# Kernel tuning notes

Hardware: AMD Instinct MI355X
Metric: run time of the kernel (lower is better)

## Reference

```python
import jax, jax.numpy as jnp
import numpy as np

EPS = 1e-5
SLOPE = 0.01  # LeakyReLU default
C = 512
C2 = C // 2
B, D, W, H = 2, 16, 16, 16


def _leaky(x):
    return jnp.where(x >= 0, x, SLOPE * x)


def _bn_c(x, g, b, rm, rv):
    # per-channel BN (eval mode) over axis 1 of a (B,C,...) tensor
    shape = (1, -1) + (1,) * (x.ndim - 2)
    inv = jax.lax.rsqrt(rv + EPS)
    return (x - rm.reshape(shape)) * (inv * g).reshape(shape) + b.reshape(shape)


def _bn_s(x, g, b, rm, rv):
    # scalar-feature BatchNorm1d(1) in eval mode
    return (x - rm[0]) * (jax.lax.rsqrt(rv[0] + EPS) * g[0]) + b[0]


def setup_inputs() -> dict:
    key = jax.random.key(0)
    ks = jax.random.split(key, 8)
    s = 0.02
    inp = {
        'x': jax.random.normal(ks[0], (B, C, D, W, H), jnp.float32),
        'topo_prompt': jax.random.normal(ks[1], (D, W, H, 6), jnp.float32) * s,
        # edge_aggregation_func: Linear(6,1)+BN1d(1)
        'w_ea': jax.random.normal(ks[2], (1, 6), jnp.float32) * s,
        'b_ea': jnp.zeros((1,), jnp.float32),
        'g_ea': jnp.ones((1,), jnp.float32), 'be_ea': jnp.zeros((1,), jnp.float32),
        'rm_ea': jnp.zeros((1,), jnp.float32), 'rv_ea': jnp.ones((1,), jnp.float32),
        # vertex_update_func: Linear(2C, C/2)+BN1d(C/2)
        'w_v': jax.random.normal(ks[3], (C2, 2 * C), jnp.float32) * s,
        'b_v': jnp.zeros((C2,), jnp.float32),
        'g_v': jnp.ones((C2,), jnp.float32), 'be_v': jnp.zeros((C2,), jnp.float32),
        'rm_v': jnp.zeros((C2,), jnp.float32), 'rv_v': jnp.ones((C2,), jnp.float32),
        # edge_update_func: Linear(2C, C/2)+BN1d(C/2)
        'w_e': jax.random.normal(ks[4], (C2, 2 * C), jnp.float32) * s,
        'b_e': jnp.zeros((C2,), jnp.float32),
        'g_e': jnp.ones((C2,), jnp.float32), 'be_e': jnp.zeros((C2,), jnp.float32),
        'rm_e': jnp.zeros((C2,), jnp.float32), 'rv_e': jnp.ones((C2,), jnp.float32),
        # update_edge_reduce_func: Linear(6,1)+BN1d(1)
        'w_r': jax.random.normal(ks[5], (1, 6), jnp.float32) * s,
        'b_r': jnp.zeros((1,), jnp.float32),
        'g_r': jnp.ones((1,), jnp.float32), 'be_r': jnp.zeros((1,), jnp.float32),
        'rm_r': jnp.zeros((1,), jnp.float32), 'rv_r': jnp.ones((1,), jnp.float32),
        # final_aggregation_layer: Conv3d(3C/2 -> C, k=1, bias=False)+BN3d(C)
        'w_f': jax.random.normal(ks[6], (C, C + C2), jnp.float32) * s,
        'g_f': jnp.ones((C,), jnp.float32), 'be_f': jnp.zeros((C,), jnp.float32),
        'rm_f': jnp.zeros((C,), jnp.float32), 'rv_f': jnp.ones((C,), jnp.float32),
    }
    return inp


def reference(x, topo_prompt,
              w_ea, b_ea, g_ea, be_ea, rm_ea, rv_ea,
              w_v, b_v, g_v, be_v, rm_v, rv_v,
              w_e, b_e, g_e, be_e, rm_e, rv_e,
              w_r, b_r, g_r, be_r, rm_r, rv_r,
              w_f, g_f, be_f, rm_f, rv_f):
    # 6-neighbor circular shifts: cat((x[-1:], x[:-1])) == roll(+1); cat((x[1:], x[:1])) == roll(-1)
    shifts = jnp.stack([
        jnp.roll(x, 1, axis=2), jnp.roll(x, -1, axis=2),
        jnp.roll(x, 1, axis=3), jnp.roll(x, -1, axis=3),
        jnp.roll(x, 1, axis=4), jnp.roll(x, -1, axis=4),
    ], axis=-1)  # (B,C,D,W,H,6)
    edge = shifts * x[..., None] + topo_prompt  # topo_prompt (D,W,H,6) broadcasts

    # edge aggregation: Linear(6->1) + BN1d(1) + LeakyReLU
    agg = jnp.einsum('bcdwhk,k->bcdwh', edge, w_ea[0]) + b_ea[0]
    agg = _leaky(_bn_s(agg, g_ea, be_ea, rm_ea, rv_ea))  # (B,C,D,W,H)

    # vertex update: Linear(2C->C/2) + BN + LeakyReLU
    feat_v = jnp.concatenate([x, agg], axis=1)  # (B,2C,D,W,H)
    uv = jnp.einsum('bcdwh,oc->bodwh', feat_v, w_v) + b_v[None, :, None, None, None]
    uv = _leaky(_bn_c(uv, g_v, be_v, rm_v, rv_v))  # (B,C/2,D,W,H)

    # edge update: cat(vertex x6, edge) on channel dim -> Linear(2C->C/2) + BN + LeakyReLU
    vrep = jnp.broadcast_to(x[..., None], x.shape + (6,))
    feat_e = jnp.concatenate([vrep, edge], axis=1)  # (B,2C,D,W,H,6)
    ue = jnp.einsum('bcdwhk,oc->bodwhk', feat_e, w_e) + b_e[None, :, None, None, None, None]
    ue = _leaky(_bn_c(ue, g_e, be_e, rm_e, rv_e))  # (B,C/2,D,W,H,6)

    # reduce 6 neighbors: Linear(6->1) + BN1d(1) + LeakyReLU
    ur = jnp.einsum('bodwhk,k->bodwh', ue, w_r[0]) + b_r[0]
    ur = _leaky(_bn_s(ur, g_r, be_r, rm_r, rv_r))  # (B,C/2,D,W,H)

    update_feature = uv * ur

    # final 1x1x1 conv (bias=False) + BN3d + LeakyReLU
    fused = jnp.concatenate([x, update_feature], axis=1)  # (B,3C/2,D,W,H)
    out = jnp.einsum('bcdwh,oc->bodwh', fused, w_f)
    out = _leaky(_bn_c(out, g_f, be_f, rm_f, rv_f))
    return out
```

## Files before the change

### kernel.cpp

```cpp
#include <hip/hip_runtime.h>

#define BATCH 2
#define C 512
#define C2 256
#define V 4096
#define NROWS 8192
#define EPS 1e-5f
#define SLOPE 0.01f
#define LDSW 40

typedef __bf16 bf16;
typedef __bf16 bf16x8 __attribute__((ext_vector_type(8)));
typedef __bf16 bf16x4 __attribute__((ext_vector_type(4)));
typedef float  f32x4  __attribute__((ext_vector_type(4)));

__device__ __forceinline__ float leaky(float x) { return x >= 0.f ? x : SLOPE * x; }

__device__ __forceinline__ int nbr(int v, int k) {
    int h = v & 15, w = (v >> 4) & 15, d = v >> 8;
    switch (k) {
        case 0: return (v & 0x0FF) | (((d + 15) & 15) << 8);
        case 1: return (v & 0x0FF) | (((d + 1) & 15) << 8);
        case 2: return (v & 0xF0F) | (((w + 15) & 15) << 4);
        case 3: return (v & 0xF0F) | (((w + 1) & 15) << 4);
        case 4: return (v & 0xFF0) | ((h + 15) & 15);
        default: return (v & 0xFF0) | ((h + 1) & 15);
    }
}

__device__ __forceinline__ void mmstep(const bf16* A, const bf16* B,
                                       f32x4 (&acc)[4][4], int abase, int bbase,
                                       int lr, int kg)
{
    bf16x8 af[4], bv[4];
    #pragma unroll
    for (int mb = 0; mb < 4; mb++)
        af[mb] = *(const bf16x8*)(A + (abase + mb * 16 + lr) * LDSW + kg * 8);
    #pragma unroll
    for (int nb = 0; nb < 4; nb++)
        bv[nb] = *(const bf16x8*)(B + (bbase + nb * 16 + lr) * LDSW + kg * 8);
    #pragma unroll
    for (int mb = 0; mb < 4; mb++)
        #pragma unroll
        for (int nb = 0; nb < 4; nb++)
            acc[mb][nb] = __builtin_amdgcn_mfma_f32_16x16x32_bf16(af[mb], bv[nb], acc[mb][nb], 0, 0, 0);
}

__global__ __launch_bounds__(256) void k_prep(
    const float* wv, const float* we, const float* wf,
    const float* w_ea, const float* b_ea, const float* g_ea, const float* be_ea,
    const float* rm_ea, const float* rv_ea,
    const float* b_v, const float* g_v, const float* be_v, const float* rm_v, const float* rv_v,
    const float* b_e, const float* g_e, const float* be_e, const float* rm_e, const float* rv_e,
    const float* w_r, const float* b_r, const float* g_r, const float* be_r,
    const float* rm_r, const float* rv_r,
    const float* g_f, const float* be_f, const float* rm_f, const float* rv_f,
    float* P, float* obv, float* obe, float* obf,
    bf16* wmain, bf16* we2, bf16* owf)
{
    int i = blockIdx.x * 256 + threadIdx.x;
    if (i < 524288) {
        int o = i >> 10, c = i & 1023;
        float val;
        if (o < 256) val = rsqrtf(rv_v[o] + EPS) * g_v[o] * wv[(size_t)o * 1024 + c];
        else {
            int oe = o - 256;
            val = (c < 512) ? rsqrtf(rv_e[oe] + EPS) * g_e[oe] * we[(size_t)oe * 1024 + c] : 0.f;
        }
        wmain[i] = (bf16)val;
    } else if (i < 655360) {
        int j = i - 524288; int o = j >> 9, c = j & 511;
        we2[j] = (bf16)(rsqrtf(rv_e[o] + EPS) * g_e[o] * we[(size_t)o * 1024 + 512 + c]);
    } else if (i < 1048576) {
        int j = i - 655360; int o = j / 768;
        owf[j] = (bf16)(rsqrtf(rv_f[o] + EPS) * g_f[o] * wf[j]);
    }
    if (blockIdx.x == 0) {
        int t = threadIdx.x;
        obf[t]       = be_f[t]       - rsqrtf(rv_f[t]       + EPS) * g_f[t]       * rm_f[t];
        obf[t + 256] = be_f[t + 256] - rsqrtf(rv_f[t + 256] + EPS) * g_f[t + 256] * rm_f[t + 256];
        float sv = rsqrtf(rv_v[t] + EPS) * g_v[t];
        obv[t] = sv * (b_v[t] - rm_v[t]) + be_v[t];
        float se = rsqrtf(rv_e[t] + EPS) * g_e[t];
        obe[t] = se * (b_e[t] - rm_e[t]) + be_e[t];
        if (t < 6) {
            float sa = rsqrtf(rv_ea[0] + EPS) * g_ea[0];
            P[t] = sa * w_ea[t];
            float sr = rsqrtf(rv_r[0] + EPS) * g_r[0];
            P[8 + t] = sr * w_r[t];
        }
        if (t == 6) {
            float sa = rsqrtf(rv_ea[0] + EPS) * g_ea[0];
            P[6] = sa * (b_ea[0] - rm_ea[0]) + be_ea[0];
            float sr = rsqrtf(rv_r[0] + EPS) * g_r[0];
            P[14] = sr * (b_r[0] - rm_r[0]) + be_r[0];
        }
    }
}

__global__ __launch_bounds__(256) void k_aggT(
    const float* __restrict__ x, const float* __restrict__ topo,
    const float* __restrict__ P,
    bf16* __restrict__ xT, bf16* __restrict__ aggT)
{
    __shared__ float T[64][65];
    const int t = threadIdx.x;
    const int b = blockIdx.z, ct = blockIdx.y * 64, vt = blockIdx.x * 64;
    const int cl = t >> 2;
    const int c  = ct + cl;
    const int vl0 = (t & 3) * 16;
    const int v0 = vt + vl0;
    const int w = (v0 >> 4) & 15, d = v0 >> 8;
    const float* xp = x + (((size_t)b * C + c) << 12);

    float xr[16], xd0[16], xd1[16], xw0[16], xw1[16];
    #pragma unroll
    for (int i = 0; i < 4; i++) {
        float4 a;
        a = ((const float4*)(xp + v0))[i];                        xr [4*i]=a.x; xr [4*i+1]=a.y; xr [4*i+2]=a.z; xr [4*i+3]=a.w;
        a = ((const float4*)(xp + (((d+15)&15)<<8) + (w<<4)))[i]; xd0[4*i]=a.x; xd0[4*i+1]=a.y; xd0[4*i+2]=a.z; xd0[4*i+3]=a.w;
        a = ((const float4*)(xp + (((d+ 1)&15)<<8) + (w<<4)))[i]; xd1[4*i]=a.x; xd1[4*i+1]=a.y; xd1[4*i+2]=a.z; xd1[4*i+3]=a.w;
        a = ((const float4*)(xp + (d<<8) + (((w+15)&15)<<4)))[i]; xw0[4*i]=a.x; xw0[4*i+1]=a.y; xw0[4*i+2]=a.z; xw0[4*i+3]=a.w;
        a = ((const float4*)(xp + (d<<8) + (((w+ 1)&15)<<4)))[i]; xw1[4*i]=a.x; xw1[4*i+1]=a.y; xw1[4*i+2]=a.z; xw1[4*i+3]=a.w;
    }

    #pragma unroll
    for (int p = 0; p < 2; ++p) {
        float val[16];
        if (p == 0) {
            #pragma unroll
            for (int j = 0; j < 16; j++) val[j] = xr[j];
        } else {
            #pragma unroll
            for (int j = 0; j < 16; j++) {
                const float* tp = topo + (size_t)(v0 + j) * 6;
                float s = P[6];
                s = fmaf(P[0], fmaf(xd0[j], xr[j], tp[0]), s);
                s = fmaf(P[1], fmaf(xd1[j], xr[j], tp[1]), s);
                s = fmaf(P[2], fmaf(xw0[j], xr[j], tp[2]), s);
                s = fmaf(P[3], fmaf(xw1[j], xr[j], tp[3]), s);
                s = fmaf(P[4], fmaf(xr[(j+15)&15], xr[j], tp[4]), s);
                s = fmaf(P[5], fmaf(xr[(j+ 1)&15], xr[j], tp[5]), s);
                val[j] = leaky(s);
            }
        }
        __syncthreads();
        #pragma unroll
        for (int j = 0; j < 16; j++) T[cl][vl0 + j] = val[j];
        __syncthreads();
        const int vr = t >> 2, c0 = (t & 3) * 16;
        bf16x8 lo, hi;
        #pragma unroll
        for (int i = 0; i < 8; i++) {
            lo[i] = (bf16)T[c0 + i][vr];
            hi[i] = (bf16)T[c0 + 8 + i][vr];
        }
        bf16* dst = (p == 0) ? xT : aggT;
        bf16* dp = dst + ((size_t)(b << 12) + vt + vr) * C + ct + c0;
        *(bf16x8*)dp = lo;
        *(bf16x8*)(dp + 8) = hi;
    }
}

template<bool MAIN>
__device__ __forceinline__ void gemm_body(
    int m0, int n0, int kk, int nsteps,
    const bf16* __restrict__ wA, int ldA,
    const bf16* __restrict__ xT, const bf16* __restrict__ aggT,
    const float* __restrict__ topo, const float* __restrict__ bvp,
    bf16* __restrict__ uvT, float* __restrict__ sxe, bf16* __restrict__ se,
    bf16 (*A)[128 * LDSW], bf16 (*B)[128 * LDSW])
{
    const int t = threadIdx.x, lane = t & 63;
    const int wv = t >> 6, wmi = wv >> 1, wni = wv & 1;
    const int lr = lane & 15, kg = lane >> 4;

    const int arow = t >> 1, acol = (t & 1) * 16;
    const bf16* pA = wA + (size_t)(m0 + arow) * ldA + acol;
    const int rB = n0 + arow;
    const bf16* pBx = xT + (size_t)rB * C + acol;
    const bf16* pB2;
    float tp = 0.f;
    if (MAIN) {
        pB2 = aggT + (size_t)rB * C + acol;
    } else {
        const int vvv = rB & 4095, bb = rB >> 12;
        pB2 = xT + (size_t)((bb << 12) | nbr(vvv, kk)) * C + acol;
        tp = topo[vvv * 6 + kk];
    }

    f32x4 acc[4][4];
    #pragma unroll
    for (int mb = 0; mb < 4; mb++)
        #pragma unroll
        for (int nb = 0; nb < 4; nb++) acc[mb][nb] = 0.f;

    uint4 a0, a1, b0, b1, n0r, n1r;
    auto issue = [&](int s) {
        a0 = *(const uint4*)(pA + s * 32);
        a1 = *(const uint4*)(pA + s * 32 + 8);
        if (MAIN) {
            const bf16* src = (s < 16) ? pBx : pB2;
            b0 = *(const uint4*)(src + (s & 15) * 32);
            b1 = *(const uint4*)(src + (s & 15) * 32 + 8);
        } else {
            b0  = *(const uint4*)(pBx + s * 32);
            b1  = *(const uint4*)(pBx + s * 32 + 8);
            n0r = *(const uint4*)(pB2 + s * 32);
            n1r = *(const uint4*)(pB2 + s * 32 + 8);
        }
    };
    auto commitStep = [&](int buf) {
        *(uint4*)(&A[buf][arow * LDSW + acol])     = a0;
        *(uint4*)(&A[buf][arow * LDSW + acol + 8]) = a1;
        if (MAIN) {
            *(uint4*)(&B[buf][arow * LDSW + acol])     = b0;
            *(uint4*)(&B[buf][arow * LDSW + acol + 8]) = b1;
        } else {
            bf16x8 xa0 = *(bf16x8*)&b0, xn0 = *(bf16x8*)&n0r;
            bf16x8 xa1 = *(bf16x8*)&b1, xn1 = *(bf16x8*)&n1r;
            bf16x8 e0, e1;
            #pragma unroll
            for (int i = 0; i < 8; i++) {
                e0[i] = (bf16)fmaf((float)xa0[i], (float)xn0[i], tp);
                e1[i] = (bf16)fmaf((float)xa1[i], (float)xn1[i], tp);
            }
            *(bf16x8*)(&B[buf][arow * LDSW + acol])     = e0;
            *(bf16x8*)(&B[buf][arow * LDSW + acol + 8]) = e1;
        }
    };

    issue(0);
    commitStep(0);
    issue(1);
    __syncthreads();
    #pragma unroll 1
    for (int s = 0; s < nsteps; ++s) {
        mmstep(A[s & 1], B[s & 1], acc, wmi * 64, wni * 64, lr, kg);
        if (s + 1 < nsteps) {
            commitStep((s + 1) & 1);
            if (s + 2 < nsteps) issue(s + 2);
            __syncthreads();
        }
    }

    if (MAIN) {
        if (m0 < 256) {
            #pragma unroll
            for (int mb = 0; mb < 4; mb++) {
                const int o = m0 + wmi * 64 + mb * 16 + kg * 4;
                f32x4 bv4 = *(const f32x4*)(bvp + o);
                #pragma unroll
                for (int nb = 0; nb < 4; nb++) {
                    const int col = n0 + wni * 64 + nb * 16 + lr;
                    bf16x4 o4;
                    #pragma unroll
                    for (int q = 0; q < 4; q++)
                        o4[q] = (bf16)leaky(acc[mb][nb][q] + bv4[q]);
                    *(bf16x4*)(uvT + (size_t)col * C2 + o) = o4;
                }
            }
        } else {
            #pragma unroll
            for (int mb = 0; mb < 4; mb++) {
                const int o = (m0 - 256) + wmi * 64 + mb * 16 + kg * 4;
                #pragma unroll
                for (int nb = 0; nb < 4; nb++) {
                    const int col = n0 + wni * 64 + nb * 16 + lr;
                    *(f32x4*)(sxe + (size_t)col * C2 + o) = acc[mb][nb];
                }
            }
        }
    } else {
        #pragma unroll
        for (int mb = 0; mb < 4; mb++) {
            const int o = m0 + wmi * 64 + mb * 16 + kg * 4;
            #pragma unroll
            for (int nb = 0; nb < 4; nb++) {
                const int col = n0 + wni * 64 + nb * 16 + lr;
                bf16x4 o4;
                #pragma unroll
                for (int q = 0; q < 4; q++) o4[q] = (bf16)acc[mb][nb][q];
                *(bf16x4*)(se + ((size_t)kk * NROWS + col) * C2 + o) = o4;
            }
        }
    }
}

__global__ __launch_bounds__(256, 3) void k_gemm(
    const bf16* __restrict__ xT, const bf16* __restrict__ aggT,
    const bf16* __restrict__ wm, const bf16* __restrict__ we2,
    const float* __restrict__ bvp, const float* __restrict__ topo,
    bf16* __restrict__ uvT, float* __restrict__ sxe, bf16* __restrict__ se)
{
    __shared__ __align__(16) bf16 A[2][128 * LDSW];
    __shared__ __align__(16) bf16 B[2][128 * LDSW];
    const int bid = (blockIdx.x & 7) * 128 + (blockIdx.x >> 3);
    if (bid < 256) {
        const int m0 = (bid & 3) * 128, n0 = (bid >> 2) * 128;
        const int nsteps = (m0 < 256) ? 32 : 16;
        gemm_body<true>(m0, n0, 0, nsteps, wm, 1024, xT, aggT, topo, bvp,
                        uvT, sxe, nullptr, A, B);
    } else {
        const int e = bid - 256;
        const int m0 = (e & 1) * 128;
        const int g = e >> 1, kk = g % 6, n0 = (g / 6) * 128;
        gemm_body<false>(m0, n0, kk, 16, we2, 512, xT, aggT, topo, bvp,
                         nullptr, nullptr, se, A, B);
    }
}

__global__ __launch_bounds__(256) void k_comb(
    const float* __restrict__ sxe, const bf16* __restrict__ se,
    const bf16* __restrict__ uvT, const float* __restrict__ bep,
    const float* __restrict__ P, bf16* __restrict__ updT)
{
    const int g = blockIdx.x * 256 + threadIdx.x;
    const int row = g >> 5, o0 = (g & 31) * 8;
    const size_t base = (size_t)row * C2 + o0;

    f32x4 sx0 = *(const f32x4*)(sxe + base);
    f32x4 sx1 = *(const f32x4*)(sxe + base + 4);
    f32x4 be0 = *(const f32x4*)(bep + o0);
    f32x4 be1 = *(const f32x4*)(bep + o0 + 4);
    float ur[8] = {};
    #pragma unroll
    for (int k = 0; k < 6; k++) {
        bf16x8 s8 = *(const bf16x8*)(se + (size_t)k * NROWS * C2 + base);
        const float wrk = P[8 + k];
        #pragma unroll
        for (int i = 0; i < 4; i++) {
            ur[i]     = fmaf(wrk, leaky(sx0[i] + (float)s8[i]     + be0[i]), ur[i]);
            ur[i + 4] = fmaf(wrk, leaky(sx1[i] + (float)s8[i + 4] + be1[i]), ur[i + 4]);
        }
    }
    const float brp = P[14];
    bf16x8 uv8 = *(const bf16x8*)(uvT + base);
    bf16x8 o8;
    #pragma unroll
    for (int i = 0; i < 8; i++)
        o8[i] = (bf16)((float)uv8[i] * leaky(ur[i] + brp));
    *(bf16x8*)(updT + base) = o8;
}

__global__ __launch_bounds__(256, 3) void k_out(
    const bf16* __restrict__ xT, const bf16* __restrict__ updT,
    const bf16* __restrict__ wf, const float* __restrict__ bfp,
    float* __restrict__ out)
{
    __shared__ __align__(16) bf16 A[2][128 * LDSW];
    __shared__ __align__(16) bf16 B[2][128 * LDSW];
    const int t = threadIdx.x, lane = t & 63;
    const int wv = t >> 6, wmi = wv >> 1, wni = wv & 1;
    const int lr = lane & 15, kg = lane >> 4;
    const int bid = (blockIdx.x & 7) * 32 + (blockIdx.x >> 3);
    const int m0 = (bid & 3) * 128, n0 = (bid >> 2) * 128;

    const int arow = t >> 1, acol = (t & 1) * 16;
    const bf16* pA = wf + (size_t)(m0 + arow) * 768 + acol;
    const bf16* pBx = xT   + (size_t)(n0 + arow) * C  + acol;
    const bf16* pBu = updT + (size_t)(n0 + arow) * C2 + acol;

    f32x4 acc[4][4];
    #pragma unroll
    for (int mb = 0; mb < 4; mb++)
        #pragma unroll
        for (int nb = 0; nb < 4; nb++) acc[mb][nb] = 0.f;

    uint4 a0, a1, b0, b1;
    auto issue = [&](int s) {
        a0 = *(const uint4*)(pA + s * 32);
        a1 = *(const uint4*)(pA + s * 32 + 8);
        const bf16* src = (s < 16) ? (pBx + s * 32) : (pBu + (s - 16) * 32);
        b0 = *(const uint4*)(src);
        b1 = *(const uint4*)(src + 8);
    };
    auto commitStep = [&](int buf) {
        *(uint4*)(&A[buf][arow * LDSW + acol])     = a0;
        *(uint4*)(&A[buf][arow * LDSW + acol + 8]) = a1;
        *(uint4*)(&B[buf][arow * LDSW + acol])     = b0;
        *(uint4*)(&B[buf][arow * LDSW + acol + 8]) = b1;
    };

    issue(0);
    commitStep(0);
    issue(1);
    __syncthreads();
    #pragma unroll 1
    for (int s = 0; s < 24; ++s) {
        mmstep(A[s & 1], B[s & 1], acc, wmi * 64, wni * 64, lr, kg);
        if (s + 1 < 24) {
            commitStep((s + 1) & 1);
            if (s + 2 < 24) issue(s + 2);
            __syncthreads();
        }
    }

    #pragma unroll
    for (int mb = 0; mb < 4; mb++) {
        const int o = m0 + wmi * 64 + mb * 16 + kg * 4;
        f32x4 bf4 = *(const f32x4*)(bfp + o);
        #pragma unroll
        for (int nb = 0; nb < 4; nb++) {
            const int col = n0 + wni * 64 + nb * 16 + lr;
            const int b = col >> 12, v = col & 4095;
            #pragma unroll
            for (int q = 0; q < 4; q++)
                out[(((size_t)b * C + o + q) << 12) + v] = leaky(acc[mb][nb][q] + bf4[q]);
        }
    }
}

extern "C" void kernel_launch(void* const* d_in, const int* in_sizes, int n_in,
                              void* d_out, int out_size, void* d_ws, size_t ws_size,
                              hipStream_t stream)
{
    const float* x    = (const float*)d_in[0];
    const float* topo = (const float*)d_in[1];
    const float* w_ea = (const float*)d_in[2];
    const float* b_ea = (const float*)d_in[3];
    const float* g_ea = (const float*)d_in[4];
    const float* be_ea= (const float*)d_in[5];
    const float* rm_ea= (const float*)d_in[6];
    const float* rv_ea= (const float*)d_in[7];
    const float* w_v  = (const float*)d_in[8];
    const float* b_v  = (const float*)d_in[9];
    const float* g_v  = (const float*)d_in[10];
    const float* be_v = (const float*)d_in[11];
    const float* rm_v = (const float*)d_in[12];
    const float* rv_v = (const float*)d_in[13];
    const float* w_e  = (const float*)d_in[14];
    const float* b_e  = (const float*)d_in[15];
    const float* g_e  = (const float*)d_in[16];
    const float* be_e = (const float*)d_in[17];
    const float* rm_e = (const float*)d_in[18];
    const float* rv_e = (const float*)d_in[19];
    const float* w_r  = (const float*)d_in[20];
    const float* b_r  = (const float*)d_in[21];
    const float* g_r  = (const float*)d_in[22];
    const float* be_r = (const float*)d_in[23];
    const float* rm_r = (const float*)d_in[24];
    const float* rv_r = (const float*)d_in[25];
    const float* w_f  = (const float*)d_in[26];
    const float* g_f  = (const float*)d_in[27];
    const float* be_f = (const float*)d_in[28];
    const float* rm_f = (const float*)d_in[29];
    const float* rv_f = (const float*)d_in[30];

    char* base = (char*)d_ws;
    size_t off = 0;
    auto take = [&](size_t bytes) { size_t r = off; off = (off + bytes + 255) & ~(size_t)255; return r; };
    float* P    = (float*)(base + take(64 * 4));
    float* bvp  = (float*)(base + take(256 * 4));
    float* bep  = (float*)(base + take(256 * 4));
    float* bfp  = (float*)(base + take(512 * 4));
    bf16*  wmp  = (bf16*)(base + take((size_t)524288 * 2));
    bf16*  we2p = (bf16*)(base + take((size_t)131072 * 2));
    bf16*  wfp  = (bf16*)(base + take((size_t)393216 * 2));
    bf16*  xT   = (bf16*)(base + take((size_t)NROWS * C * 2));
    bf16*  aggT = (bf16*)(base + take((size_t)NROWS * C * 2));
    bf16*  uvT  = (bf16*)(base + take((size_t)NROWS * C2 * 2));
    bf16*  updT = (bf16*)(base + take((size_t)NROWS * C2 * 2));
    float* sxe  = (float*)(base + take((size_t)NROWS * C2 * 4));
    bf16*  se   = (bf16*)(base + take((size_t)6 * NROWS * C2 * 2));

    k_prep<<<4096, 256, 0, stream>>>(
        w_v, w_e, w_f,
        w_ea, b_ea, g_ea, be_ea, rm_ea, rv_ea,
        b_v, g_v, be_v, rm_v, rv_v,
        b_e, g_e, be_e, rm_e, rv_e,
        w_r, b_r, g_r, be_r, rm_r, rv_r,
        g_f, be_f, rm_f, rv_f,
        P, bvp, bep, bfp, wmp, we2p, wfp);

    k_aggT<<<dim3(64, 8, 2), 256, 0, stream>>>(x, topo, P, xT, aggT);

    k_gemm<<<dim3(1024), 256, 0, stream>>>(xT, aggT, wmp, we2p, bvp, topo, uvT, sxe, se);
    k_comb<<<dim3(NROWS * C2 / 8 / 256), 256, 0, stream>>>(sxe, se, uvT, bep, P, updT);
    k_out<<<dim3(256), 256, 0, stream>>>(xT, updT, wfp, bfp, (float*)d_out);
}
```

Before: 104.2 us.

## Stage GEMM tiles directly into LDS with global_load_lds and drop block swizzle

Operand tiles in the weight-side and plain-activation GEMM paths are now copied straight from global memory into LDS with the global_load_lds builtin, instead of going through registers. This changes the LDS layout to an unpadded 32-element row stride and restructures the double-buffered loop so the next stage is issued right after the barrier. The edge path keeps its register-computed B tile with padding. The blockIdx swizzle in both GEMM kernels is also removed. The aim is to free VGPRs and drop the LDS write instructions, but the unpadded layout can cause LDS bank conflicts on the MFMA fragment reads, and dropping the swizzle can change L2 locality.

```diff
diff --git a/kernel.cpp b/kernel.cpp
--- a/kernel.cpp
+++ b/kernel.cpp
@@ -7,7 +7,7 @@
 #define NROWS 8192
 #define EPS 1e-5f
 #define SLOPE 0.01f
-#define LDSW 40
+#define BPAD 40
 
 typedef __bf16 bf16;
 typedef __bf16 bf16x8 __attribute__((ext_vector_type(8)));
@@ -28,6 +28,23 @@
     }
 }
 
+__device__ __forceinline__ void gload16(const bf16* g, bf16* l) {
+    __builtin_amdgcn_global_load_lds(
+        (const __attribute__((address_space(1))) void*)g,
+        (__attribute__((address_space(3))) void*)l, 16, 0, 0);
+}
+
+__device__ __forceinline__ void stage_gl(bf16* buf, const bf16* srcbase, size_t ld,
+                                         int kcol, int wv, int lane) {
+    #pragma unroll
+    for (int j = 0; j < 2; j++) {
+        const int rl = wv * 32 + j * 16;
+        gload16(srcbase + (size_t)(rl + (lane >> 2)) * ld + kcol + (lane & 3) * 8,
+                buf + rl * 32);
+    }
+}
+
+template<int SA, int SB>
 __device__ __forceinline__ void mmstep(const bf16* A, const bf16* B,
                                        f32x4 (&acc)[4][4], int abase, int bbase,
                                        int lr, int kg)
@@ -35,10 +52,10 @@
     bf16x8 af[4], bv[4];
     #pragma unroll
     for (int mb = 0; mb < 4; mb++)
-        af[mb] = *(const bf16x8*)(A + (abase + mb * 16 + lr) * LDSW + kg * 8);
+        af[mb] = *(const bf16x8*)(A + (abase + mb * 16 + lr) * SA + kg * 8);
     #pragma unroll
     for (int nb = 0; nb < 4; nb++)
-        bv[nb] = *(const bf16x8*)(B + (bbase + nb * 16 + lr) * LDSW + kg * 8);
+        bv[nb] = *(const bf16x8*)(B + (bbase + nb * 16 + lr) * SB + kg * 8);
     #pragma unroll
     for (int mb = 0; mb < 4; mb++)
         #pragma unroll
@@ -165,27 +182,27 @@
 template<bool MAIN>
 __device__ __forceinline__ void gemm_body(
     int m0, int n0, int kk, int nsteps,
-    const bf16* __restrict__ wA, int ldA,
+    const bf16* __restrict__ wA, size_t ldA,
     const bf16* __restrict__ xT, const bf16* __restrict__ aggT,
     const float* __restrict__ topo, const float* __restrict__ bvp,
     bf16* __restrict__ uvT, float* __restrict__ sxe, bf16* __restrict__ se,
-    bf16 (*A)[128 * LDSW], bf16 (*B)[128 * LDSW])
+    bf16 (*A)[128 * 32], bf16 (*B)[128 * BPAD])
 {
     const int t = threadIdx.x, lane = t & 63;
     const int wv = t >> 6, wmi = wv >> 1, wni = wv & 1;
     const int lr = lane & 15, kg = lane >> 4;
 
-    const int arow = t >> 1, acol = (t & 1) * 16;
-    const bf16* pA = wA + (size_t)(m0 + arow) * ldA + acol;
-    const int rB = n0 + arow;
-    const bf16* pBx = xT + (size_t)rB * C + acol;
-    const bf16* pB2;
-    float tp = 0.f;
-    if (MAIN) {
-        pB2 = aggT + (size_t)rB * C + acol;
-    } else {
+    const bf16* wAb  = wA + (size_t)m0 * ldA;
+    const bf16* xTb  = xT + (size_t)n0 * C;
+    const bf16* agTb = aggT + (size_t)n0 * C;
+
+    const int erow = t >> 1, ecol = (t & 1) * 16;
+    const bf16* pBx = nullptr; const bf16* pB2 = nullptr; float tp = 0.f;
+    if (!MAIN) {
+        const int rB = n0 + erow;
         const int vvv = rB & 4095, bb = rB >> 12;
-        pB2 = xT + (size_t)((bb << 12) | nbr(vvv, kk)) * C + acol;
+        pBx = xT + (size_t)rB * C + ecol;
+        pB2 = xT + (size_t)((bb << 12) | nbr(vvv, kk)) * C + ecol;
         tp = topo[vvv * 6 + kk];
     }
 
@@ -195,53 +212,48 @@
         #pragma unroll
         for (int nb = 0; nb < 4; nb++) acc[mb][nb] = 0.f;
 
-    uint4 a0, a1, b0, b1, n0r, n1r;
-    auto issue = [&](int s) {
-        a0 = *(const uint4*)(pA + s * 32);
-        a1 = *(const uint4*)(pA + s * 32 + 8);
+    uint4 b0, b1, n0r, n1r;
+    auto issueB = [&](int s) {
+        b0  = *(const uint4*)(pBx + s * 32);
+        b1  = *(const uint4*)(pBx + s * 32 + 8);
+        n0r = *(const uint4*)(pB2 + s * 32);
+        n1r = *(const uint4*)(pB2 + s * 32 + 8);
+    };
+    auto commitB = [&](int buf) {
+        bf16x8 xa0 = *(bf16x8*)&b0, xn0 = *(bf16x8*)&n0r;
+        bf16x8 xa1 = *(bf16x8*)&b1, xn1 = *(bf16x8*)&n1r;
+        bf16x8 e0, e1;
+        #pragma unroll
+        for (int i = 0; i < 8; i++) {
+            e0[i] = (bf16)fmaf((float)xa0[i], (float)xn0[i], tp);
+            e1[i] = (bf16)fmaf((float)xa1[i], (float)xn1[i], tp);
+        }
+        *(bf16x8*)(&B[buf][erow * BPAD + ecol])     = e0;
+        *(bf16x8*)(&B[buf][erow * BPAD + ecol + 8]) = e1;
+    };
+    auto stageStep = [&](int buf, int s) {
+        stage_gl(A[buf], wAb, ldA, s * 32, wv, lane);
         if (MAIN) {
-            const bf16* src = (s < 16) ? pBx : pB2;
-            b0 = *(const uint4*)(src + (s & 15) * 32);
-            b1 = *(const uint4*)(src + (s & 15) * 32 + 8);
-        } else {
-            b0  = *(const uint4*)(pBx + s * 32);
-            b1  = *(const uint4*)(pBx + s * 32 + 8);
-            n0r = *(const uint4*)(pB2 + s * 32);
-            n1r = *(const uint4*)(pB2 + s * 32 + 8);
+            if (s < 16) stage_gl(B[buf], xTb, C, s * 32, wv, lane);
+            else        stage_gl(B[buf], agTb, C, (s - 16) * 32, wv, lane);
         }
     };
-    auto commitStep = [&](int buf) {
-        *(uint4*)(&A[buf][arow * LDSW + acol])     = a0;
-        *(uint4*)(&A[buf][arow * LDSW + acol + 8]) = a1;
-        if (MAIN) {
-            *(uint4*)(&B[buf][arow * LDSW + acol])     = b0;
-            *(uint4*)(&B[buf][arow * LDSW + acol + 8]) = b1;
-        } else {
-            bf16x8 xa0 = *(bf16x8*)&b0, xn0 = *(bf16x8*)&n0r;
-            bf16x8 xa1 = *(bf16x8*)&b1, xn1 = *(bf16x8*)&n1r;
-            bf16x8 e0, e1;
-            #pragma unroll
-            for (int i = 0; i < 8; i++) {
-                e0[i] = (bf16)fmaf((float)xa0[i], (float)xn0[i], tp);
-                e1[i] = (bf16)fmaf((float)xa1[i], (float)xn1[i], tp);
-            }
-            *(bf16x8*)(&B[buf][arow * LDSW + acol])     = e0;
-            *(bf16x8*)(&B[buf][arow * LDSW + acol + 8]) = e1;
-        }
-    };
-
-    issue(0);
-    commitStep(0);
-    issue(1);
-    __syncthreads();
+
+    stageStep(0, 0);
+    if (!MAIN) { issueB(0); commitB(0); if (nsteps > 1) issueB(1); }
+
+    int cb = 0;
     #pragma unroll 1
     for (int s = 0; s < nsteps; ++s) {
-        mmstep(A[s & 1], B[s & 1], acc, wmi * 64, wni * 64, lr, kg);
-        if (s + 1 < nsteps) {
-            commitStep((s + 1) & 1);
-            if (s + 2 < nsteps) issue(s + 2);
-            __syncthreads();
-        }
+        __syncthreads();
+        if (s + 1 < nsteps) stageStep(cb ^ 1, s + 1);
+        if (MAIN) mmstep<32, 32>(A[cb], B[cb], acc, wmi * 64, wni * 64, lr, kg);
+        else      mmstep<32, BPAD>(A[cb], B[cb], acc, wmi * 64, wni * 64, lr, kg);
+        if (!MAIN && s + 1 < nsteps) {
+            commitB(cb ^ 1);
+            if (s + 2 < nsteps) issueB(s + 2);
+        }
+        cb ^= 1;
     }
 
     if (MAIN) {
@@ -293,9 +305,9 @@
     const float* __restrict__ bvp, const float* __restrict__ topo,
     bf16* __restrict__ uvT, float* __restrict__ sxe, bf16* __restrict__ se)
 {
-    __shared__ __align__(16) bf16 A[2][128 * LDSW];
-    __shared__ __align__(16) bf16 B[2][128 * LDSW];
-    const int bid = (blockIdx.x & 7) * 128 + (blockIdx.x >> 3);
+    __shared__ __align__(16) bf16 A[2][128 * 32];
+    __shared__ __align__(16) bf16 B[2][128 * BPAD];
+    const int bid = blockIdx.x;
     if (bid < 256) {
         const int m0 = (bid & 3) * 128, n0 = (bid >> 2) * 128;
         const int nsteps = (m0 < 256) ? 32 : 16;
@@ -348,18 +360,17 @@
     const bf16* __restrict__ wf, const float* __restrict__ bfp,
     float* __restrict__ out)
 {
-    __shared__ __align__(16) bf16 A[2][128 * LDSW];
-    __shared__ __align__(16) bf16 B[2][128 * LDSW];
+    __shared__ __align__(16) bf16 A[2][128 * 32];
+    __shared__ __align__(16) bf16 B[2][128 * 32];
     const int t = threadIdx.x, lane = t & 63;
     const int wv = t >> 6, wmi = wv >> 1, wni = wv & 1;
     const int lr = lane & 15, kg = lane >> 4;
-    const int bid = (blockIdx.x & 7) * 32 + (blockIdx.x >> 3);
+    const int bid = blockIdx.x;
     const int m0 = (bid & 3) * 128, n0 = (bid >> 2) * 128;
 
-    const int arow = t >> 1, acol = (t & 1) * 16;
-    const bf16* pA = wf + (size_t)(m0 + arow) * 768 + acol;
-    const bf16* pBx = xT   + (size_t)(n0 + arow) * C  + acol;
-    const bf16* pBu = updT + (size_t)(n0 + arow) * C2 + acol;
+    const bf16* wAb = wf   + (size_t)m0 * 768;
+    const bf16* xTb = xT   + (size_t)n0 * C;
+    const bf16* uTb = updT + (size_t)n0 * C2;
 
     f32x4 acc[4][4];
     #pragma unroll
@@ -367,33 +378,20 @@
         #pragma unroll
         for (int nb = 0; nb < 4; nb++) acc[mb][nb] = 0.f;
 
-    uint4 a0, a1, b0, b1;
-    auto issue = [&](int s) {
-        a0 = *(const uint4*)(pA + s * 32);
-        a1 = *(const uint4*)(pA + s * 32 + 8);
-        const bf16* src = (s < 16) ? (pBx + s * 32) : (pBu + (s - 16) * 32);
-        b0 = *(const uint4*)(src);
-        b1 = *(const uint4*)(src + 8);
+    auto stageStep = [&](int buf, int s) {
+        stage_gl(A[buf], wAb, 768, s * 32, wv, lane);
+        if (s < 16) stage_gl(B[buf], xTb, C, s * 32, wv, lane);
+        else        stage_gl(B[buf], uTb, C2, (s - 16) * 32, wv, lane);
     };
-    auto commitStep = [&](int buf) {
-        *(uint4*)(&A[buf][arow * LDSW + acol])     = a0;
-        *(uint4*)(&A[buf][arow * LDSW + acol + 8]) = a1;
-        *(uint4*)(&B[buf][arow * LDSW + acol])     = b0;
-        *(uint4*)(&B[buf][arow * LDSW + acol + 8]) = b1;
-    };
-
-    issue(0);
-    commitStep(0);
-    issue(1);
-    __syncthreads();
+
+    stageStep(0, 0);
+    int cb = 0;
     #pragma unroll 1
     for (int s = 0; s < 24; ++s) {
-        mmstep(A[s & 1], B[s & 1], acc, wmi * 64, wni * 64, lr, kg);
-        if (s + 1 < 24) {
-            commitStep((s + 1) & 1);
-            if (s + 2 < 24) issue(s + 2);
-            __syncthreads();
-        }
+        __syncthreads();
+        if (s + 1 < 24) stageStep(cb ^ 1, s + 1);
+        mmstep<32, 32>(A[cb], B[cb], acc, wmi * 64, wni * 64, lr, kg);
+        cb ^= 1;
     }
 
     #pragma unroll
```

New measurement: 99.38 us. -4.6%, faster.
